# Kernel tuning notes

Measured on AMD Instinct MI355X. Metric: run time of the kernel, lower is better.

The kernel has to match this reference:

```python
import jax, jax.numpy as jnp
import numpy as np

INF = 1.0e12
B, L, D, H = 8, 128, 512, 8
DV = D // H

def _xavier(key, shape, fan_in, fan_out):
    a = float(np.sqrt(6.0 / (fan_in + fan_out)))
    return jax.random.uniform(key, shape, jnp.float32, -a, a)

def setup_inputs() -> dict:
    key = jax.random.key(0)
    ks = jax.random.split(key, 12)
    inp = jax.random.normal(ks[0], (B, L, D), jnp.float32)
    relation_inp = jax.random.normal(ks[1], (B, L, L, D), jnp.float32)
    mask = jnp.zeros((B, L, L), dtype=bool)  # no padding masked
    adj_mask = jax.random.randint(ks[2], (B, H, L, L), 0, 2).astype(jnp.int32)
    idx = jnp.arange(L)
    adj_mask = adj_mask.at[:, :, idx, idx].set(1)  # ensure non-empty neighborhoods
    rel_pos_mat = jnp.zeros((B, L, L), jnp.int32)
    deprel_mat = jnp.zeros((B, L, L), jnp.int32)
    deparc_mat = jnp.zeros((B, L, L), jnp.int32)
    W_value = _xavier(ks[3], (D, H * DV), D, H * DV)
    W_relation = _xavier(ks[4], (D, H * DV), D, H * DV)
    # weight vectors have torch shape (1,1,1,H,DV); xavier fan over last 2 dims
    w_src = _xavier(ks[5], (H, DV), H, DV)
    w_tgt = _xavier(ks[6], (H, DV), H, DV)
    w_rel = _xavier(ks[7], (H, DV), H, DV)
    W_final = _xavier(ks[8], (2 * D, D), 2 * D, D)
    b_final = jnp.zeros((D,), jnp.float32)
    return {"inp": inp, "relation_inp": relation_inp, "mask": mask,
            "adj_mask": adj_mask, "rel_pos_mat": rel_pos_mat,
            "deprel_mat": deprel_mat, "deparc_mat": deparc_mat,
            "W_value": W_value, "W_relation": W_relation,
            "w_src": w_src, "w_tgt": w_tgt, "w_rel": w_rel,
            "W_final": W_final, "b_final": b_final}

def _leaky(x):
    return jnp.where(x >= 0, x, 0.2 * x)

def reference(inp, relation_inp, mask, adj_mask, rel_pos_mat, deprel_mat,
              deparc_mat, W_value, W_relation, w_src, w_tgt, w_rel,
              W_final, b_final):
    b, l, d = inp.shape
    h, dv = w_src.shape
    # value: [B,H,L,DV]
    value = (inp @ W_value).reshape(b, l, h, dv).transpose(0, 2, 1, 3)
    # additive GAT scores without materializing [B,L,L,H,DV] src/tgt tensors
    e_src = jnp.einsum('bhld,hd->bhl', value, w_src)  # source index j
    e_tgt = jnp.einsum('bhld,hd->bhl', value, w_tgt)  # target index i
    scores_value = _leaky(e_tgt[:, :, :, None] + e_src[:, :, None, :])  # [B,H,L,L]
    # relation projection: [B,L,L,H,DV]
    relation = (relation_inp @ W_relation).reshape(b, l, l, h, dv)
    scores_relation = _leaky(jnp.einsum('bijhd,hd->bhij', relation, w_rel))
    # masks
    pad = mask[:, None]                       # [B,1,L,L] True = masked
    noadj = adj_mask == 0                     # [B,H,L,L]
    bad = pad | noadj
    scores_value = jnp.where(bad, -INF, scores_value)
    scores_relation = jnp.where(bad, -INF, scores_relation)
    attn_value = jax.nn.softmax(scores_value, axis=-1)
    attn_relation = jax.nn.softmax(scores_relation, axis=-1)
    # normalized: multiply by 1/adj (0 where no edge since adj in {0,1}), L1 renorm
    adjf = adj_mask.astype(attn_value.dtype)
    def renorm(a):
        a = a * adjf
        s = jnp.sum(jnp.abs(a), axis=-1, keepdims=True)
        return a / jnp.maximum(s, 1e-12)
    attn_value = renorm(attn_value)
    attn_relation = renorm(attn_relation)
    # zero masked / non-adjacent entries
    attn_value = jnp.where(bad, 0.0, attn_value)
    attn_relation = jnp.where(bad, 0.0, attn_relation)
    out_v = jnp.einsum('bhij,bhjd->bhid', attn_value, value)
    out_r = jnp.einsum('bhij,bhjd->bhid', attn_relation, value)
    out_v = out_v.transpose(0, 2, 1, 3).reshape(b, l, h * dv)
    out_r = out_r.transpose(0, 2, 1, 3).reshape(b, l, h * dv)
    final = jnp.concatenate([out_v, out_r], axis=-1) @ W_final + b_final
    final = final + inp
    return final, attn_value, attn_relation
```

## Files before the change

### kernel.cpp

```cpp
#include <hip/hip_runtime.h>

#define B_ 8
#define L_ 128
#define D_ 512
#define H_ 8

__device__ __forceinline__ float leaky(float v) { return fmaxf(v, 0.2f * v); }

__global__ __launch_bounds__(256) void k_wreff(const float* __restrict__ Wrel,
                                               const float* __restrict__ wrel,
                                               float* __restrict__ wr_eff) {
    int t = blockIdx.x * 256 + threadIdx.x;
    int k = t >> 3, h = t & 7;
    const float4* a = (const float4*)(Wrel + k * 512 + h * 64);
    const float4* b = (const float4*)(wrel + h * 64);
    float acc = 0.f;
#pragma unroll
    for (int q = 0; q < 16; q++) {
        float4 av = a[q], bv = b[q];
        acc += av.x * bv.x + av.y * bv.y + av.z * bv.z + av.w * bv.w;
    }
    wr_eff[k * 8 + h] = acc;
}

__global__ __launch_bounds__(256) void k_srel_value(
        const float* __restrict__ rel, const float* __restrict__ wr_eff,
        const float* __restrict__ inp, const float* __restrict__ Wv,
        const float* __restrict__ wsrc, const float* __restrict__ wtgt,
        float* __restrict__ s_rel, float* __restrict__ value_t,
        float* __restrict__ e_src, float* __restrict__ e_tgt) {
    __shared__ float xs[4][512];
    const int t = threadIdx.x;

    if (blockIdx.x < 2048) {
        const int lane = t & 63;
        const int wave = (blockIdx.x * 256 + t) >> 6;

        float wrl[64];
        {
            const float4* wp = (const float4*)(wr_eff + lane * 64);
#pragma unroll
            for (int q = 0; q < 16; q++) {
                float4 v = wp[q];
                wrl[q * 4 + 0] = v.x; wrl[q * 4 + 1] = v.y;
                wrl[q * 4 + 2] = v.z; wrl[q * 4 + 3] = v.w;
            }
        }

        const bool hi32 = (lane & 32) != 0;
        const bool hi16 = (lane & 16) != 0;
        const bool hi8  = (lane & 8) != 0;
        const int  hsel = (lane >> 3) & 7;

#pragma unroll 2
        for (int it = 0; it < 16; ++it) {
            int row = wave + it * 8192;
            const float4* rp = (const float4*)(rel + (size_t)row * 512 + lane * 8);
            float4 u0 = rp[0];
            float4 u1 = rp[1];
            float x[8];
            x[0] = u0.x; x[1] = u0.y; x[2] = u0.z; x[3] = u0.w;
            x[4] = u1.x; x[5] = u1.y; x[6] = u1.z; x[7] = u1.w;
            float acc[8] = {0.f,0.f,0.f,0.f,0.f,0.f,0.f,0.f};
#pragma unroll
            for (int kk = 0; kk < 8; kk++)
#pragma unroll
                for (int h = 0; h < 8; h++)
                    acc[h] = fmaf(x[kk], wrl[kk * 8 + h], acc[h]);

            float a4[4];
#pragma unroll
            for (int hh = 0; hh < 4; hh++) {
                float send = hi32 ? acc[hh] : acc[hh + 4];
                float recv = __shfl_xor(send, 32, 64);
                float own  = hi32 ? acc[hh + 4] : acc[hh];
                a4[hh] = own + recv;
            }
            float a2[2];
#pragma unroll
            for (int hh = 0; hh < 2; hh++) {
                float send = hi16 ? a4[hh] : a4[hh + 2];
                float recv = __shfl_xor(send, 16, 64);
                float own  = hi16 ? a4[hh + 2] : a4[hh];
                a2[hh] = own + recv;
            }
            float send = hi8 ? a2[0] : a2[1];
            float recv = __shfl_xor(send, 8, 64);
            float a1 = (hi8 ? a2[1] : a2[0]) + recv;
            a1 += __shfl_xor(a1, 4, 64);
            a1 += __shfl_xor(a1, 2, 64);
            a1 += __shfl_xor(a1, 1, 64);

            if ((lane & 7) == 0) {
                float v = leaky(a1);
                int b = row >> 14, rem = row & 16383;
                s_rel[(((size_t)(b * 8 + hsel)) << 14) + rem] = v;
            }
        }
        return;
    }

    const int row0 = (blockIdx.x - 2048) * 4;
    {
        int r = t >> 6, seg = t & 63;
        const float4* ip = (const float4*)(inp + (size_t)(row0 + r) * 512 + seg * 8);
        float4 a = ip[0], bq = ip[1];
        *(float4*)&xs[r][seg * 8]     = a;
        *(float4*)&xs[r][seg * 8 + 4] = bq;
    }
    __syncthreads();
    const int c0 = t * 2;
    float acc[4][2] = {};
    for (int k0 = 0; k0 < 512; k0 += 4) {
        float4 xr[4];
#pragma unroll
        for (int r = 0; r < 4; r++) xr[r] = *(const float4*)&xs[r][k0];
#define VSTEP(COMP, I)                                                          \
        {                                                                       \
            float2 wv = *(const float2*)(Wv + (size_t)(k0 + I) * 512 + c0);     \
            _Pragma("unroll")                                                   \
            for (int r = 0; r < 4; r++) {                                       \
                acc[r][0] = fmaf(xr[r].COMP, wv.x, acc[r][0]);                  \
                acc[r][1] = fmaf(xr[r].COMP, wv.y, acc[r][1]);                  \
            }                                                                   \
        }
        VSTEP(x, 0) VSTEP(y, 1) VSTEP(z, 2) VSTEP(w, 3)
#undef VSTEP
    }
    const int h = t >> 5;
    const int d0 = c0 & 63;
    const int b = row0 >> 7, l0 = row0 & 127;
    {
        float4 v0 = make_float4(acc[0][0], acc[1][0], acc[2][0], acc[3][0]);
        float4 v1 = make_float4(acc[0][1], acc[1][1], acc[2][1], acc[3][1]);
        *(float4*)&value_t[((size_t)((b * 8 + h) * 64 + d0)) * 128 + l0] = v0;
        *(float4*)&value_t[((size_t)((b * 8 + h) * 64 + d0 + 1)) * 128 + l0] = v1;
    }
    float ws0 = wsrc[c0], ws1 = wsrc[c0 + 1];
    float wt0 = wtgt[c0], wt1 = wtgt[c0 + 1];
    float es[4], et[4];
#pragma unroll
    for (int r = 0; r < 4; r++) {
        es[r] = acc[r][0] * ws0 + acc[r][1] * ws1;
        et[r] = acc[r][0] * wt0 + acc[r][1] * wt1;
    }
#pragma unroll
    for (int off = 16; off >= 1; off >>= 1)
#pragma unroll
        for (int r = 0; r < 4; r++) {
            es[r] += __shfl_xor(es[r], off, 64);
            et[r] += __shfl_xor(et[r], off, 64);
        }
    if ((t & 31) == 0) {
#pragma unroll
        for (int r = 0; r < 4; r++) {
            e_src[(b * 8 + h) * 128 + l0 + r] = es[r];
            e_tgt[(b * 8 + h) * 128 + l0 + r] = et[r];
        }
    }
}

__global__ __launch_bounds__(256) void k_attn_final(
        const float* s_rel, const float* __restrict__ value_t,
        const float* __restrict__ e_src, const float* __restrict__ e_tgt,
        const int* __restrict__ adj, const unsigned char* __restrict__ mask,
        const float* __restrict__ Wf, const float* __restrict__ bias,
        const float* __restrict__ inp,
        float* __restrict__ out_av, float* out_ar, float* __restrict__ outf) {
    __shared__ float xls[4][1024];
    __shared__ float lav[4][128];
    __shared__ float lar[4][128];
    const int t = threadIdx.x;
    const int lane = t & 63;
    const int w = t >> 6;
    const int b = blockIdx.x >> 5;
    const int iq = blockIdx.x & 31;
    const int i = iq * 4 + w;
    const int j0 = lane, j1 = lane + 64;

    const unsigned char m0 = mask[(size_t)(b * 128 + i) * 128 + j0];
    const unsigned char m1 = mask[(size_t)(b * 128 + i) * 128 + j1];

    for (int h = 0; h < 8; h++) {
        const int bh = b * 8 + h;
        const size_t rowbase = ((size_t)bh * 128 + i) * 128;
        const float etg = e_tgt[bh * 128 + i];

        float sv0 = leaky(etg + e_src[bh * 128 + j0]);
        float sv1 = leaky(etg + e_src[bh * 128 + j1]);
        float sr0 = s_rel[rowbase + j0];
        float sr1 = s_rel[rowbase + j1];
        int a0 = adj[rowbase + j0], a1 = adj[rowbase + j1];
        bool bad0 = m0 || (a0 == 0);
        bool bad1 = m1 || (a1 == 0);
        if (bad0) { sv0 = -1e30f; sr0 = -1e30f; }
        if (bad1) { sv1 = -1e30f; sr1 = -1e30f; }

        float mv = fmaxf(sv0, sv1), mr = fmaxf(sr0, sr1);
#pragma unroll
        for (int off = 32; off >= 1; off >>= 1) {
            mv = fmaxf(mv, __shfl_xor(mv, off, 64));
            mr = fmaxf(mr, __shfl_xor(mr, off, 64));
        }
        float pv0 = bad0 ? 0.f : __expf(sv0 - mv);
        float pv1 = bad1 ? 0.f : __expf(sv1 - mv);
        float pr0 = bad0 ? 0.f : __expf(sr0 - mr);
        float pr1 = bad1 ? 0.f : __expf(sr1 - mr);
        float sumv = pv0 + pv1, sumr = pr0 + pr1;
#pragma unroll
        for (int off = 32; off >= 1; off >>= 1) {
            sumv += __shfl_xor(sumv, off, 64);
            sumr += __shfl_xor(sumr, off, 64);
        }
        float iv = 1.f / fmaxf(sumv, 1e-12f);
        float ir = 1.f / fmaxf(sumr, 1e-12f);
        float av0 = pv0 * iv, av1 = pv1 * iv;
        float ar0 = pr0 * ir, ar1 = pr1 * ir;

        out_av[rowbase + j0] = av0;
        out_av[rowbase + j1] = av1;
        out_ar[rowbase + j0] = ar0;
        out_ar[rowbase + j1] = ar1;

        lav[w][j0] = av0; lav[w][j1] = av1;
        lar[w][j0] = ar0; lar[w][j1] = ar1;

        const float4* vrow = (const float4*)(value_t + ((size_t)bh * 64 + lane) * 128);
        float accv = 0.f, accr = 0.f;
#pragma unroll 8
        for (int jb = 0; jb < 32; jb++) {
            float4 v4 = vrow[jb];
            float4 a4 = *(const float4*)&lav[w][jb * 4];
            float4 r4 = *(const float4*)&lar[w][jb * 4];
            accv = fmaf(a4.x, v4.x, accv); accv = fmaf(a4.y, v4.y, accv);
            accv = fmaf(a4.z, v4.z, accv); accv = fmaf(a4.w, v4.w, accv);
            accr = fmaf(r4.x, v4.x, accr); accr = fmaf(r4.y, v4.y, accr);
            accr = fmaf(r4.z, v4.z, accr); accr = fmaf(r4.w, v4.w, accr);
        }
        xls[w][h * 64 + lane] = accv;
        xls[w][512 + h * 64 + lane] = accr;
    }
    __syncthreads();

    const int c0 = t * 2;
    float acc[4][2] = {};
    for (int k0 = 0; k0 < 1024; k0 += 4) {
        float4 xr[4];
#pragma unroll
        for (int r = 0; r < 4; r++) xr[r] = *(const float4*)&xls[r][k0];
#define FSTEP(COMP, I)                                                          \
        {                                                                       \
            float2 wv = *(const float2*)(Wf + (size_t)(k0 + I) * 512 + c0);     \
            _Pragma("unroll")                                                   \
            for (int r = 0; r < 4; r++) {                                       \
                acc[r][0] = fmaf(xr[r].COMP, wv.x, acc[r][0]);                  \
                acc[r][1] = fmaf(xr[r].COMP, wv.y, acc[r][1]);                  \
            }                                                                   \
        }
        FSTEP(x, 0) FSTEP(y, 1) FSTEP(z, 2) FSTEP(w, 3)
#undef FSTEP
    }
    const int row0 = blockIdx.x * 4;
    float b0 = bias[c0], b1 = bias[c0 + 1];
#pragma unroll
    for (int r = 0; r < 4; r++) {
        size_t ro = (size_t)(row0 + r) * 512;
        float2 ivl = *(const float2*)(inp + ro + c0);
        float v0 = acc[r][0] + b0 + ivl.x;
        float v1 = acc[r][1] + b1 + ivl.y;
        *(float2*)&outf[ro + c0] = make_float2(v0, v1);
    }
}

extern "C" void kernel_launch(void* const* d_in, const int* in_sizes, int n_in,
                              void* d_out, int out_size, void* d_ws, size_t ws_size,
                              hipStream_t stream) {
    const float* inp  = (const float*)d_in[0];
    const float* rel  = (const float*)d_in[1];
    const unsigned char* mask = (const unsigned char*)d_in[2];
    const int*   adj  = (const int*)d_in[3];
    const float* Wv   = (const float*)d_in[7];
    const float* Wr   = (const float*)d_in[8];
    const float* wsrc = (const float*)d_in[9];
    const float* wtgt = (const float*)d_in[10];
    const float* wrel = (const float*)d_in[11];
    const float* Wf   = (const float*)d_in[12];
    const float* bfin = (const float*)d_in[13];

    float* outf   = (float*)d_out;
    float* out_av = outf + (size_t)B_ * L_ * D_;
    float* out_ar = out_av + (size_t)B_ * H_ * L_ * L_;

    char* ws = (char*)d_ws;
    float* wr_eff  = (float*)(ws);
    float* value_t = (float*)(ws + 16384);
    float* e_src   = (float*)(ws + 2113536);
    float* e_tgt   = (float*)(ws + 2146304);

    k_wreff<<<16, 256, 0, stream>>>(Wr, wrel, wr_eff);
    k_srel_value<<<2304, 256, 0, stream>>>(rel, wr_eff, inp, Wv, wsrc, wtgt,
                                           out_ar, value_t, e_src, e_tgt);
    k_attn_final<<<256, 256, 0, stream>>>(out_ar, value_t, e_src, e_tgt, adj, mask,
                                          Wf, bfin, inp, out_av, out_ar, outf);
}
```

Baseline: 533.4 us.

## Double attention-final block width and split heads and GEMM K across halves

```diff
diff --git a/kernel.cpp b/kernel.cpp
--- a/kernel.cpp
+++ b/kernel.cpp
@@ -54,7 +54,7 @@
 
 #pragma unroll 2
         for (int it = 0; it < 16; ++it) {
-            int row = wave + it * 8192;
+            int row = wave * 16 + it;
             const float4* rp = (const float4*)(rel + (size_t)row * 512 + lane * 8);
             float4 u0 = rp[0];
             float4 u1 = rp[1];
@@ -160,7 +160,7 @@
     }
 }
 
-__global__ __launch_bounds__(256) void k_attn_final(
+__global__ __launch_bounds__(512) void k_attn_final(
         const float* s_rel, const float* __restrict__ value_t,
         const float* __restrict__ e_src, const float* __restrict__ e_tgt,
         const int* __restrict__ adj, const unsigned char* __restrict__ mask,
@@ -168,20 +168,24 @@
         const float* __restrict__ inp,
         float* __restrict__ out_av, float* out_ar, float* __restrict__ outf) {
     __shared__ float xls[4][1024];
-    __shared__ float lav[4][128];
-    __shared__ float lar[4][128];
+    __shared__ float ltmp[2048];
     const int t = threadIdx.x;
     const int lane = t & 63;
     const int w = t >> 6;
+    const int r = w >> 1;
+    const int hh = w & 1;
     const int b = blockIdx.x >> 5;
     const int iq = blockIdx.x & 31;
-    const int i = iq * 4 + w;
+    const int i = iq * 4 + r;
     const int j0 = lane, j1 = lane + 64;
+    float* lav = &ltmp[w * 256];
+    float* lar = lav + 128;
 
     const unsigned char m0 = mask[(size_t)(b * 128 + i) * 128 + j0];
     const unsigned char m1 = mask[(size_t)(b * 128 + i) * 128 + j1];
 
-    for (int h = 0; h < 8; h++) {
+    for (int h8 = 0; h8 < 4; h8++) {
+        const int h = hh * 4 + h8;
         const int bh = b * 8 + h;
         const size_t rowbase = ((size_t)bh * 128 + i) * 128;
         const float etg = e_tgt[bh * 128 + i];
@@ -222,53 +226,65 @@
         out_ar[rowbase + j0] = ar0;
         out_ar[rowbase + j1] = ar1;
 
-        lav[w][j0] = av0; lav[w][j1] = av1;
-        lar[w][j0] = ar0; lar[w][j1] = ar1;
+        lav[j0] = av0; lav[j1] = av1;
+        lar[j0] = ar0; lar[j1] = ar1;
 
         const float4* vrow = (const float4*)(value_t + ((size_t)bh * 64 + lane) * 128);
         float accv = 0.f, accr = 0.f;
 #pragma unroll 8
         for (int jb = 0; jb < 32; jb++) {
             float4 v4 = vrow[jb];
-            float4 a4 = *(const float4*)&lav[w][jb * 4];
-            float4 r4 = *(const float4*)&lar[w][jb * 4];
+            float4 a4 = *(const float4*)&lav[jb * 4];
+            float4 r4 = *(const float4*)&lar[jb * 4];
             accv = fmaf(a4.x, v4.x, accv); accv = fmaf(a4.y, v4.y, accv);
             accv = fmaf(a4.z, v4.z, accv); accv = fmaf(a4.w, v4.w, accv);
             accr = fmaf(r4.x, v4.x, accr); accr = fmaf(r4.y, v4.y, accr);
             accr = fmaf(r4.z, v4.z, accr); accr = fmaf(r4.w, v4.w, accr);
         }
-        xls[w][h * 64 + lane] = accv;
-        xls[w][512 + h * 64 + lane] = accr;
+        xls[r][h * 64 + lane] = accv;
+        xls[r][512 + h * 64 + lane] = accr;
     }
     __syncthreads();
 
-    const int c0 = t * 2;
+    const int g  = t >> 8;
+    const int tt = t & 255;
+    const int c0 = tt * 2;
+    const int kb = g * 512;
     float acc[4][2] = {};
-    for (int k0 = 0; k0 < 1024; k0 += 4) {
+    for (int k0 = 0; k0 < 512; k0 += 4) {
         float4 xr[4];
 #pragma unroll
-        for (int r = 0; r < 4; r++) xr[r] = *(const float4*)&xls[r][k0];
+        for (int rr = 0; rr < 4; rr++) xr[rr] = *(const float4*)&xls[rr][kb + k0];
 #define FSTEP(COMP, I)                                                          \
         {                                                                       \
-            float2 wv = *(const float2*)(Wf + (size_t)(k0 + I) * 512 + c0);     \
+            float2 wv = *(const float2*)(Wf + (size_t)(kb + k0 + I) * 512 + c0);\
             _Pragma("unroll")                                                   \
-            for (int r = 0; r < 4; r++) {                                       \
-                acc[r][0] = fmaf(xr[r].COMP, wv.x, acc[r][0]);                  \
-                acc[r][1] = fmaf(xr[r].COMP, wv.y, acc[r][1]);                  \
+            for (int rr = 0; rr < 4; rr++) {                                    \
+                acc[rr][0] = fmaf(xr[rr].COMP, wv.x, acc[rr][0]);               \
+                acc[rr][1] = fmaf(xr[rr].COMP, wv.y, acc[rr][1]);               \
             }                                                                   \
         }
         FSTEP(x, 0) FSTEP(y, 1) FSTEP(z, 2) FSTEP(w, 3)
 #undef FSTEP
     }
-    const int row0 = blockIdx.x * 4;
-    float b0 = bias[c0], b1 = bias[c0 + 1];
-#pragma unroll
-    for (int r = 0; r < 4; r++) {
-        size_t ro = (size_t)(row0 + r) * 512;
-        float2 ivl = *(const float2*)(inp + ro + c0);
-        float v0 = acc[r][0] + b0 + ivl.x;
-        float v1 = acc[r][1] + b1 + ivl.y;
-        *(float2*)&outf[ro + c0] = make_float2(v0, v1);
+    if (g == 1) {
+#pragma unroll
+        for (int rr = 0; rr < 4; rr++)
+            *(float2*)&ltmp[rr * 512 + c0] = make_float2(acc[rr][0], acc[rr][1]);
+    }
+    __syncthreads();
+    if (g == 0) {
+        const int row0 = blockIdx.x * 4;
+        float b0 = bias[c0], b1 = bias[c0 + 1];
+#pragma unroll
+        for (int rr = 0; rr < 4; rr++) {
+            size_t ro = (size_t)(row0 + rr) * 512;
+            float2 p   = *(const float2*)&ltmp[rr * 512 + c0];
+            float2 ivl = *(const float2*)(inp + ro + c0);
+            float v0 = acc[rr][0] + p.x + b0 + ivl.x;
+            float v1 = acc[rr][1] + p.y + b1 + ivl.y;
+            *(float2*)&outf[ro + c0] = make_float2(v0, v1);
+        }
     }
 }
 
@@ -300,6 +316,6 @@
     k_wreff<<<16, 256, 0, stream>>>(Wr, wrel, wr_eff);
     k_srel_value<<<2304, 256, 0, stream>>>(rel, wr_eff, inp, Wv, wsrc, wtgt,
                                            out_ar, value_t, e_src, e_tgt);
-    k_attn_final<<<256, 256, 0, stream>>>(out_ar, value_t, e_src, e_tgt, adj, mask,
+    k_attn_final<<<256, 512, 0, stream>>>(out_ar, value_t, e_src, e_tgt, adj, mask,
                                           Wf, bfin, inp, out_av, out_ar, outf);
 }
```

Measured after the change: 495.2 us. -7.2%, faster.
